# Optimization experiments

Hardware: AMD Instinct MI355X
Metric: run time of the kernel (lower is better)

The kernel has to match this reference:

```python
import jax, jax.numpy as jnp
import numpy as np

B, V = 4, 5                      # batch_size, nview
CUBE = (80, 80, 20)              # PICT_STRUCT.CUBE_SIZE
NBINS = CUBE[0] * CUBE[1] * CUBE[2]
IMG_W, IMG_H = 960, 512          # NETWORK.IMAGE_SIZE (w, h)
ORI_W, ORI_H = 1920, 1080        # NETWORK.ORI_IMAGE_SIZE
HM_W, HM_H = 240, 128            # NETWORK.HEATMAP_SIZE
C_IMG, C_FEAT = 3, 32
C_TOT = C_IMG + C_FEAT
HID = 256
D_IN = 3 + 2 * C_TOT             # points + [mean, var] volume features


def setup_inputs():
    key = jax.random.key(0)
    ks = jax.random.split(key, 10)
    denorm_imgs = jax.random.uniform(ks[0], (V, B, C_IMG, IMG_H, IMG_W), jnp.float32)
    feats2d = jax.random.normal(ks[1], (V, B, C_FEAT, HM_H, HM_W), jnp.float32)
    lo = jnp.array([-1500.0, -1500.0, -300.0], jnp.float32)
    hi = jnp.array([1500.0, 1500.0, 300.0], jnp.float32)
    grids = lo + (hi - lo) * jax.random.uniform(ks[2], (B, NBINS, 3), jnp.float32)
    # near-identity rotations, camera centers ~3m behind the volume so all
    # points project inside the original image
    R = jnp.tile(jnp.eye(3, dtype=jnp.float32), (V, B, 1, 1)) \
        + 0.01 * jax.random.normal(ks[3], (V, B, 3, 3), jnp.float32)
    T = jnp.tile(jnp.array([0.0, 0.0, -3000.0], jnp.float32).reshape(3, 1), (V, B, 1, 1)) \
        + 50.0 * jax.random.normal(ks[4], (V, B, 3, 1), jnp.float32)
    f = 1500.0 + 10.0 * jax.random.normal(ks[5], (V, B, 2), jnp.float32)
    c_cam = jnp.tile(jnp.array([ORI_W / 2.0, ORI_H / 2.0], jnp.float32), (V, B, 1))
    k_dist = jnp.zeros((V, B, 3), jnp.float32)
    p_dist = jnp.zeros((V, B, 2), jnp.float32)
    resize_transform = jnp.array([[IMG_W / ORI_W, 0.0, 0.0],
                                  [0.0, IMG_H / ORI_H, 0.0]], jnp.float32)
    s1, s2 = 1.0 / np.sqrt(D_IN), 1.0 / np.sqrt(HID)
    W1 = (s1 * jax.random.normal(ks[6], (D_IN, HID))).astype(jnp.float32)
    b1 = jnp.zeros((HID,), jnp.float32)
    W2 = (s2 * jax.random.normal(ks[7], (HID, HID))).astype(jnp.float32)
    b2 = jnp.zeros((HID,), jnp.float32)
    W3 = (s2 * jax.random.normal(ks[8], (HID, 1))).astype(jnp.float32)
    b3 = jnp.zeros((1,), jnp.float32)
    return dict(denorm_imgs=denorm_imgs, feats2d=feats2d, grids=grids, R=R, T=T,
                f=f, c_cam=c_cam, k_dist=k_dist, p_dist=p_dist,
                resize_transform=resize_transform,
                W1=W1, b1=b1, W2=W2, b2=b2, W3=W3, b3=b3)


def _project(x, R, T, f, c, k, p):
    # voxelpose project_point_radial: x [N,3] world-mm -> [N,2] pixel coords
    xcam = R @ (x.T - T)                               # [3,N]
    y = xcam[:2] / (xcam[2:3] + 1e-5)                  # [2,N]
    r2 = jnp.sum(y * y, axis=0)
    radial = 1.0 + k[0] * r2 + k[1] * r2 ** 2 + k[2] * r2 ** 3
    tan = p[0] * y[1] + p[1] * y[0]
    y = y * (radial + 2.0 * tan)[None, :] + jnp.stack([p[1], p[0]])[:, None] * r2[None, :]
    return (f[:, None] * y + c[:, None]).T             # [N,2]


def _bilinear(img, gx, gy):
    # F.grid_sample bilinear, align_corners=True, padding_mode='zeros'
    # img: [C,H,W]; gx,gy: [N] in [-1,1] -> [C,N]
    C, H, W = img.shape
    x = (gx + 1.0) * 0.5 * (W - 1)
    y = (gy + 1.0) * 0.5 * (H - 1)
    x0, y0 = jnp.floor(x), jnp.floor(y)
    wx1, wy1 = x - x0, y - y0
    wx0, wy0 = 1.0 - wx1, 1.0 - wy1

    def tap(xi, yi):
        valid = (xi >= 0) & (xi <= W - 1) & (yi >= 0) & (yi <= H - 1)
        xi_c = jnp.clip(xi.astype(jnp.int32), 0, W - 1)
        yi_c = jnp.clip(yi.astype(jnp.int32), 0, H - 1)
        return img[:, yi_c, xi_c] * valid.astype(img.dtype)

    return (tap(x0, y0) * (wx0 * wy0) + tap(x0 + 1.0, y0) * (wx1 * wy0)
            + tap(x0, y0 + 1.0) * (wx0 * wy1) + tap(x0 + 1.0, y0 + 1.0) * (wx1 * wy1))


def _sample_view(img, feat, pts, R, T, f, c, k, p, trans):
    xy = _project(pts, R, T, f, c, k, p)
    xy = jnp.clip(xy, -1.0, float(max(ORI_W, ORI_H)))
    xy = jnp.concatenate([xy, jnp.ones((xy.shape[0], 1), xy.dtype)], axis=1) @ trans.T
    g = xy / jnp.array([IMG_W - 1.0, IMG_H - 1.0], jnp.float32) * 2.0 - 1.0
    si = _bilinear(img, g[:, 0], g[:, 1])              # [C_IMG, N]
    sf = _bilinear(feat, g[:, 0], g[:, 1])             # [C_FEAT, N]
    return jnp.concatenate([si, sf], axis=0)           # [C_TOT, N]


def reference(denorm_imgs, feats2d, grids, R, T, f, c_cam, k_dist, p_dist,
              resize_transform, W1, b1, W2, b2, W3, b3):
    per_b = jax.vmap(_sample_view, in_axes=(0, 0, 0, 0, 0, 0, 0, 0, 0, None))
    per_vb = jax.vmap(per_b, in_axes=(0, 0, None, 0, 0, 0, 0, 0, 0, None))
    cubes = per_vb(denorm_imgs, feats2d, grids, R, T, f, c_cam, k_dist, p_dist,
                   resize_transform)                   # [V,B,C,N]
    cubes = jnp.transpose(cubes, (1, 2, 3, 0))         # [B,C,N,V]
    mean = jnp.mean(cubes, axis=-1)                    # sum(cubes/nview)
    var = jnp.sum((cubes - mean[..., None]) ** 2, axis=-1) / V
    var = jnp.exp(-var)
    gvol = jnp.concatenate([mean, var], axis=1)        # [B,2C,N]
    # nerf_model.query_density: MLP over (points, per-point global volume feats)
    feat = jnp.concatenate([grids / 1000.0, jnp.swapaxes(gvol, 1, 2)], axis=-1)  # [B,N,D_IN]
    h = jax.nn.relu(feat @ W1 + b1)
    h = jax.nn.relu(h @ W2 + b2)
    density = jax.nn.softplus(h @ W3 + b3)             # [B,N,1]
    alpha = 1.0 - jnp.exp(-density)
    return alpha.reshape(B, 1, CUBE[0], CUBE[1], CUBE[2])
```

## Files before the change

kernel.cpp:

```cpp
#include <hip/hip_runtime.h>

#define NVIEW 5
#define BATCH 4
#define NPTS 128000
#define CIMG 3
#define CFEAT 32
#define CTOT 35
#define DIN 73
#define HID 256
#define IMG_W 960
#define IMG_H 512
#define HM_W 240
#define HM_H 128
#define HW_IMG (IMG_W * IMG_H)
#define HW_HM (HM_W * HM_H)

#define BP 32

typedef __attribute__((ext_vector_type(8))) short bf16x8;
typedef __attribute__((ext_vector_type(4))) float f32x4;
typedef __attribute__((ext_vector_type(4))) unsigned short ushort4v;
typedef __attribute__((ext_vector_type(8))) unsigned short ushort8v;

__device__ inline unsigned short bf16_rtne(float f) {
    unsigned u = __builtin_bit_cast(unsigned, f);
    u += 0x7FFFu + ((u >> 16) & 1u);
    return (unsigned short)(u >> 16);
}
__device__ inline float bf2f(unsigned short u) {
    return __builtin_bit_cast(float, ((unsigned)u) << 16);
}

struct Tap {
    int o00, o01, o10, o11;
    float w00, w01, w10, w11;
};

__device__ inline void make_tap(float gx, float gy, int W, int H, Tap& t) {
    float x = (gx + 1.0f) * 0.5f * (float)(W - 1);
    float y = (gy + 1.0f) * 0.5f * (float)(H - 1);
    float x0 = floorf(x), y0 = floorf(y);
    float x1 = x0 + 1.0f, y1 = y0 + 1.0f;
    float wx1 = x - x0, wy1 = y - y0;
    float wx0 = 1.0f - wx1, wy0 = 1.0f - wy1;
    float vx0 = (x0 >= 0.0f && x0 <= (float)(W - 1)) ? 1.0f : 0.0f;
    float vx1 = (x1 >= 0.0f && x1 <= (float)(W - 1)) ? 1.0f : 0.0f;
    float vy0 = (y0 >= 0.0f && y0 <= (float)(H - 1)) ? 1.0f : 0.0f;
    float vy1 = (y1 >= 0.0f && y1 <= (float)(H - 1)) ? 1.0f : 0.0f;
    int ix0 = min(max((int)x0, 0), W - 1);
    int ix1 = min(max((int)x1, 0), W - 1);
    int iy0 = min(max((int)y0, 0), H - 1);
    int iy1 = min(max((int)y1, 0), H - 1);
    t.o00 = iy0 * W + ix0;  t.w00 = wx0 * wy0 * vx0 * vy0;
    t.o01 = iy0 * W + ix1;  t.w01 = wx1 * wy0 * vx1 * vy0;
    t.o10 = iy1 * W + ix0;  t.w10 = wx0 * wy1 * vx0 * vy1;
    t.o11 = iy1 * W + ix1;  t.w11 = wx1 * wy1 * vx1 * vy1;
}

__device__ inline float4 f4zero() { float4 r; r.x = r.y = r.z = r.w = 0.f; return r; }
__device__ inline float4 tapacc(ushort4v a, float w, float4 acc) {
    acc.x += w * bf2f(a[0]); acc.y += w * bf2f(a[1]);
    acc.z += w * bf2f(a[2]); acc.w += w * bf2f(a[3]); return acc;
}
__device__ inline float4 f4add(float4 a, float4 b) {
    a.x += b.x; a.y += b.y; a.z += b.z; a.w += b.w; return a;
}
__device__ inline float4 f4addsq(float4 acc, float4 v) {
    acc.x += v.x * v.x; acc.y += v.y * v.y; acc.z += v.z * v.z; acc.w += v.w * v.w; return acc;
}

__global__ __launch_bounds__(256) void transpose_img(const float* __restrict__ in,
                                                     unsigned short* __restrict__ out) {
    int idx = blockIdx.x * 256 + threadIdx.x;
    int vb = idx / (HW_IMG / 4);
    int p4 = idx - vb * (HW_IMG / 4);
    const float* src = in + (size_t)vb * 3 * HW_IMG + p4 * 4;
    float4 c0 = *reinterpret_cast<const float4*>(src);
    float4 c1 = *reinterpret_cast<const float4*>(src + HW_IMG);
    float4 c2 = *reinterpret_cast<const float4*>(src + 2 * HW_IMG);
    ushort8v o01, o23;
    o01[0] = bf16_rtne(c0.x); o01[1] = bf16_rtne(c1.x); o01[2] = bf16_rtne(c2.x); o01[3] = 0;
    o01[4] = bf16_rtne(c0.y); o01[5] = bf16_rtne(c1.y); o01[6] = bf16_rtne(c2.y); o01[7] = 0;
    o23[0] = bf16_rtne(c0.z); o23[1] = bf16_rtne(c1.z); o23[2] = bf16_rtne(c2.z); o23[3] = 0;
    o23[4] = bf16_rtne(c0.w); o23[5] = bf16_rtne(c1.w); o23[6] = bf16_rtne(c2.w); o23[7] = 0;
    ushort8v* dst = reinterpret_cast<ushort8v*>(out + ((size_t)vb * HW_IMG + p4 * 4) * 4);
    dst[0] = o01;
    dst[1] = o23;
}

__global__ __launch_bounds__(256) void transpose_feat(const float* __restrict__ in,
                                                      unsigned short* __restrict__ out) {
    int idx = blockIdx.x * 256 + threadIdx.x;
    int vb = idx / HW_HM;
    int pix = idx - vb * HW_HM;
    const float* src = in + (size_t)vb * 32 * HW_HM + pix;
    ushort8v* dst = reinterpret_cast<ushort8v*>(out + (size_t)idx * 32);
#pragma unroll
    for (int k = 0; k < 4; ++k) {
        ushort8v o;
#pragma unroll
        for (int j = 0; j < 8; ++j)
            o[j] = bf16_rtne(src[(8 * k + j) * HW_HM]);
        dst[k] = o;
    }
}

__global__ __launch_bounds__(256) void prep_weights(const float* __restrict__ W1,
                                                    const float* __restrict__ W2,
                                                    unsigned short* __restrict__ W1b,
                                                    unsigned short* __restrict__ W2b) {
    int idx = blockIdx.x * 256 + threadIdx.x;
    if (idx < 16 * 3 * 64) {
        int l = idx & 63;
        int ks = (idx >> 6) % 3;
        int nt = idx / 192;
        int n = nt * 16 + (l & 15);
        int k0 = ks * 32 + (l >> 4) * 8;
        ushort8v o;
#pragma unroll
        for (int j = 0; j < 8; ++j) {
            int k = k0 + j;
            float v = (k < DIN) ? W1[k * HID + n] : 0.0f;
            o[j] = bf16_rtne(v);
        }
        reinterpret_cast<ushort8v*>(W1b)[idx] = o;
    } else if (idx < 16 * 3 * 64 + 16 * 8 * 64) {
        int id2 = idx - 16 * 3 * 64;
        int l = id2 & 63;
        int ks = (id2 >> 6) & 7;
        int nt = id2 >> 9;
        int n = nt * 16 + (l & 15);
        int k0 = ks * 32 + (l >> 4) * 8;
        ushort8v o;
#pragma unroll
        for (int j = 0; j < 8; ++j)
            o[j] = bf16_rtne(W2[(k0 + j) * HID + n]);
        reinterpret_cast<ushort8v*>(W2b)[id2] = o;
    }
}

__global__ __launch_bounds__(256, 4) void fused_denorm_project(
    const unsigned short* __restrict__ wsImg,
    const unsigned short* __restrict__ wsFeat,
    const unsigned short* __restrict__ W1b,
    const unsigned short* __restrict__ W2b,
    const float* __restrict__ grids,
    const float* __restrict__ Rm,
    const float* __restrict__ Tm,
    const float* __restrict__ fcam,
    const float* __restrict__ ccam,
    const float* __restrict__ kdist,
    const float* __restrict__ pdist,
    const float* __restrict__ trans,
    const float* __restrict__ b1,
    const float* __restrict__ b2,
    const float* __restrict__ W3,
    const float* __restrict__ b3,
    float* __restrict__ out)
{
    __shared__ unsigned short featb[BP * 96];
    __shared__ unsigned short h1T[BP * 256];
    __shared__ float b1L[HID], b2L[HID], w3L[HID];
    __shared__ float partial[4][BP];

    const int tid = threadIdx.x;
    const int blk = blockIdx.x;
    const int b   = blk / (NPTS / BP);
    const int n0  = (blk % (NPTS / BP)) * BP;

    b1L[tid] = b1[tid];
    b2L[tid] = b2[tid];
    w3L[tid] = W3[tid];

    {
        const int t = tid & 7;
        const int p = tid >> 3;
        const int n = n0 + p;
        char* fbB = (char*)featb;
        const int rowoff = p * 192;
        const int sw = (p & 7) << 4;

        const float px = grids[(b * NPTS + n) * 3 + 0];
        const float py = grids[(b * NPTS + n) * 3 + 1];
        const float pz = grids[(b * NPTS + n) * 3 + 2];
        if (t == 1) {
            *(unsigned short*)(fbB + ((rowoff + 0) ^ sw)) = bf16_rtne(px * 1e-3f);
            *(unsigned short*)(fbB + ((rowoff + 2) ^ sw)) = bf16_rtne(py * 1e-3f);
            *(unsigned short*)(fbB + ((rowoff + 4) ^ sw)) = bf16_rtne(pz * 1e-3f);
        }
        {
            int c0 = 73 + t * 3;
            int cnt = (t == 7) ? 2 : 3;
            for (int j = 0; j < cnt; ++j)
                *(unsigned short*)(fbB + ((rowoff + (c0 + j) * 2) ^ sw)) = 0;
        }

        Tap myF = {}; Tap myI = {};
        if (t < NVIEW) {
            const int vb = t * BATCH + b;
            const float* Rp = Rm + vb * 9;
            const float* Tp = Tm + vb * 3;
            float X = px - Tp[0], Y = py - Tp[1], Z = pz - Tp[2];
            float xc = Rp[0] * X + Rp[1] * Y + Rp[2] * Z;
            float yc = Rp[3] * X + Rp[4] * Y + Rp[5] * Z;
            float zc = Rp[6] * X + Rp[7] * Y + Rp[8] * Z;
            float inv = 1.0f / (zc + 1e-5f);
            float y0 = xc * inv, y1 = yc * inv;
            float r2 = y0 * y0 + y1 * y1;
            float k0 = kdist[vb * 3 + 0], k1 = kdist[vb * 3 + 1], k2 = kdist[vb * 3 + 2];
            float p0 = pdist[vb * 2 + 0], p1 = pdist[vb * 2 + 1];
            float radial = 1.0f + r2 * (k0 + r2 * (k1 + r2 * k2));
            float tn = p0 * y1 + p1 * y0;
            float scl = radial + 2.0f * tn;
            float uu = y0 * scl + p1 * r2;
            float vv = y1 * scl + p0 * r2;
            float xo = fcam[vb * 2 + 0] * uu + ccam[vb * 2 + 0];
            float yo = fcam[vb * 2 + 1] * vv + ccam[vb * 2 + 1];
            xo = fminf(fmaxf(xo, -1.0f), 1920.0f);
            yo = fminf(fmaxf(yo, -1.0f), 1920.0f);
            float xr = trans[0] * xo + trans[1] * yo + trans[2];
            float yr = trans[3] * xo + trans[4] * yo + trans[5];
            float gx = xr * (1.0f / (float)(IMG_W - 1)) * 2.0f - 1.0f;
            float gy = yr * (1.0f / (float)(IMG_H - 1)) * 2.0f - 1.0f;
            make_tap(gx, gy, HM_W, HM_H, myF);
            make_tap(gx, gy, IMG_W, IMG_H, myI);
        }

        float4 s4 = f4zero(), q4 = f4zero();
        const int lb = (tid & 63) & 56;
        for (int v = 0; v < NVIEW; ++v) {
            const int src = lb + v;
            Tap tF;
            tF.o00 = __shfl(myF.o00, src, 64);
            tF.o01 = __shfl(myF.o01, src, 64);
            tF.o10 = __shfl(myF.o10, src, 64);
            tF.o11 = __shfl(myF.o11, src, 64);
            tF.w00 = __shfl(myF.w00, src, 64);
            tF.w01 = __shfl(myF.w01, src, 64);
            tF.w10 = __shfl(myF.w10, src, 64);
            tF.w11 = __shfl(myF.w11, src, 64);
            const unsigned short* fb = wsFeat + (size_t)(v * BATCH + b) * HW_HM * 32 + t * 4;
            ushort4v a00 = *reinterpret_cast<const ushort4v*>(fb + (size_t)tF.o00 * 32);
            ushort4v a01 = *reinterpret_cast<const ushort4v*>(fb + (size_t)tF.o01 * 32);
            ushort4v a10 = *reinterpret_cast<const ushort4v*>(fb + (size_t)tF.o10 * 32);
            ushort4v a11 = *reinterpret_cast<const ushort4v*>(fb + (size_t)tF.o11 * 32);
            float4 val = f4zero();
            val = tapacc(a00, tF.w00, val);
            val = tapacc(a01, tF.w01, val);
            val = tapacc(a10, tF.w10, val);
            val = tapacc(a11, tF.w11, val);
            s4 = f4add(s4, val);
            q4 = f4addsq(q4, val);
        }

        float4 si = f4zero(), qi = f4zero();
        if (t < NVIEW) {
            const unsigned short* ib = wsImg + (size_t)(t * BATCH + b) * HW_IMG * 4;
            ushort4v i00 = *reinterpret_cast<const ushort4v*>(ib + (size_t)myI.o00 * 4);
            ushort4v i01 = *reinterpret_cast<const ushort4v*>(ib + (size_t)myI.o01 * 4);
            ushort4v i10 = *reinterpret_cast<const ushort4v*>(ib + (size_t)myI.o10 * 4);
            ushort4v i11 = *reinterpret_cast<const ushort4v*>(ib + (size_t)myI.o11 * 4);
            float4 vi = f4zero();
            vi = tapacc(i00, myI.w00, vi);
            vi = tapacc(i01, myI.w01, vi);
            vi = tapacc(i10, myI.w10, vi);
            vi = tapacc(i11, myI.w11, vi);
            si = vi;
            qi = f4addsq(f4zero(), vi);
        }
#pragma unroll
        for (int off = 1; off <= 4; off <<= 1) {
            si.x += __shfl_xor(si.x, off, 64);
            si.y += __shfl_xor(si.y, off, 64);
            si.z += __shfl_xor(si.z, off, 64);
            qi.x += __shfl_xor(qi.x, off, 64);
            qi.y += __shfl_xor(qi.y, off, 64);
            qi.z += __shfl_xor(qi.z, off, 64);
        }

        const float inv5 = 1.0f / (float)NVIEW;
        {
            float m0 = s4.x * inv5, m1 = s4.y * inv5, m2 = s4.z * inv5, m3 = s4.w * inv5;
            int cm = 6 + 4 * t;
            int cv = 41 + 4 * t;
            *(unsigned short*)(fbB + ((rowoff + (cm + 0) * 2) ^ sw)) = bf16_rtne(m0);
            *(unsigned short*)(fbB + ((rowoff + (cm + 1) * 2) ^ sw)) = bf16_rtne(m1);
            *(unsigned short*)(fbB + ((rowoff + (cm + 2) * 2) ^ sw)) = bf16_rtne(m2);
            *(unsigned short*)(fbB + ((rowoff + (cm + 3) * 2) ^ sw)) = bf16_rtne(m3);
            *(unsigned short*)(fbB + ((rowoff + (cv + 0) * 2) ^ sw)) = bf16_rtne(expf(-(q4.x * inv5 - m0 * m0)));
            *(unsigned short*)(fbB + ((rowoff + (cv + 1) * 2) ^ sw)) = bf16_rtne(expf(-(q4.y * inv5 - m1 * m1)));
            *(unsigned short*)(fbB + ((rowoff + (cv + 2) * 2) ^ sw)) = bf16_rtne(expf(-(q4.z * inv5 - m2 * m2)));
            *(unsigned short*)(fbB + ((rowoff + (cv + 3) * 2) ^ sw)) = bf16_rtne(expf(-(q4.w * inv5 - m3 * m3)));
        }
        if (t == 0) {
            float m0 = si.x * inv5, m1 = si.y * inv5, m2 = si.z * inv5;
            *(unsigned short*)(fbB + ((rowoff + 3 * 2) ^ sw)) = bf16_rtne(m0);
            *(unsigned short*)(fbB + ((rowoff + 4 * 2) ^ sw)) = bf16_rtne(m1);
            *(unsigned short*)(fbB + ((rowoff + 5 * 2) ^ sw)) = bf16_rtne(m2);
            *(unsigned short*)(fbB + ((rowoff + 38 * 2) ^ sw)) = bf16_rtne(expf(-(qi.x * inv5 - m0 * m0)));
            *(unsigned short*)(fbB + ((rowoff + 39 * 2) ^ sw)) = bf16_rtne(expf(-(qi.y * inv5 - m1 * m1)));
            *(unsigned short*)(fbB + ((rowoff + 40 * 2) ^ sw)) = bf16_rtne(expf(-(qi.z * inv5 - m2 * m2)));
        }
    }
    __syncthreads();

    const int l   = tid & 63;
    const int w   = tid >> 6;
    const int g   = l >> 4;
    const int c16 = l & 15;

    {
        f32x4 acc[4][2];
#pragma unroll
        for (int nl = 0; nl < 4; ++nl)
#pragma unroll
            for (int pt = 0; pt < 2; ++pt) acc[nl][pt] = (f32x4)0.0f;

        const bf16x8* wfrag = reinterpret_cast<const bf16x8*>(W1b);
#pragma unroll
        for (int ks = 0; ks < 3; ++ks) {
            bf16x8 bfr[2];
#pragma unroll
            for (int pt = 0; pt < 2; ++pt) {
                int p = pt * 16 + c16;
                int off = (p * 192 + (ks * 32 + g * 8) * 2) ^ ((p & 7) << 4);
                bfr[pt] = *reinterpret_cast<const bf16x8*>((const char*)featb + off);
            }
#pragma unroll
            for (int nl = 0; nl < 4; ++nl) {
                int nt = w * 4 + nl;
                bf16x8 a = wfrag[(nt * 3 + ks) * 64 + l];
                acc[nl][0] = __builtin_amdgcn_mfma_f32_16x16x32_bf16(a, bfr[0], acc[nl][0], 0, 0, 0);
                acc[nl][1] = __builtin_amdgcn_mfma_f32_16x16x32_bf16(a, bfr[1], acc[nl][1], 0, 0, 0);
            }
        }
#pragma unroll
        for (int nl = 0; nl < 4; ++nl) {
            int nb = (w * 4 + nl) * 16 + g * 4;
            float bb0 = b1L[nb + 0], bb1 = b1L[nb + 1], bb2 = b1L[nb + 2], bb3v = b1L[nb + 3];
#pragma unroll
            for (int pt = 0; pt < 2; ++pt) {
                int p = pt * 16 + c16;
                ushort4v pk;
                pk[0] = bf16_rtne(fmaxf(acc[nl][pt][0] + bb0, 0.0f));
                pk[1] = bf16_rtne(fmaxf(acc[nl][pt][1] + bb1, 0.0f));
                pk[2] = bf16_rtne(fmaxf(acc[nl][pt][2] + bb2, 0.0f));
                pk[3] = bf16_rtne(fmaxf(acc[nl][pt][3] + bb3v, 0.0f));
                int off = (p * 512 + nb * 2) ^ ((p & 7) << 4);
                *reinterpret_cast<ushort4v*>((char*)h1T + off) = pk;
            }
        }
    }
    __syncthreads();

    {
        f32x4 acc[4][2];
#pragma unroll
        for (int nl = 0; nl < 4; ++nl)
#pragma unroll
            for (int pt = 0; pt < 2; ++pt) acc[nl][pt] = (f32x4)0.0f;

        const bf16x8* wfrag = reinterpret_cast<const bf16x8*>(W2b);
#pragma unroll
        for (int ks = 0; ks < 8; ++ks) {
            bf16x8 bfr[2];
#pragma unroll
            for (int pt = 0; pt < 2; ++pt) {
                int p = pt * 16 + c16;
                int off = (p * 512 + (ks * 32 + g * 8) * 2) ^ ((p & 7) << 4);
                bfr[pt] = *reinterpret_cast<const bf16x8*>((const char*)h1T + off);
            }
#pragma unroll
            for (int nl = 0; nl < 4; ++nl) {
                int nt = w * 4 + nl;
                bf16x8 a = wfrag[(nt * 8 + ks) * 64 + l];
                acc[nl][0] = __builtin_amdgcn_mfma_f32_16x16x32_bf16(a, bfr[0], acc[nl][0], 0, 0, 0);
                acc[nl][1] = __builtin_amdgcn_mfma_f32_16x16x32_bf16(a, bfr[1], acc[nl][1], 0, 0, 0);
            }
        }
        float s0 = 0.0f, s1 = 0.0f;
#pragma unroll
        for (int nl = 0; nl < 4; ++nl) {
            int nb = (w * 4 + nl) * 16 + g * 4;
#pragma unroll
            for (int r = 0; r < 4; ++r) {
                float b2v = b2L[nb + r];
                float w3v = w3L[nb + r];
                s0 += fmaxf(acc[nl][0][r] + b2v, 0.0f) * w3v;
                s1 += fmaxf(acc[nl][1][r] + b2v, 0.0f) * w3v;
            }
        }
        s0 += __shfl_xor(s0, 16, 64);
        s0 += __shfl_xor(s0, 32, 64);
        s1 += __shfl_xor(s1, 16, 64);
        s1 += __shfl_xor(s1, 32, 64);
        if (g == 0) {
            partial[w][c16]      = s0;
            partial[w][16 + c16] = s1;
        }
    }
    __syncthreads();

    if (tid < BP) {
        float v = partial[0][tid] + partial[1][tid] + partial[2][tid] + partial[3][tid] + b3[0];
        out[b * NPTS + n0 + tid] = 1.0f / (1.0f + expf(-v));
    }
}

extern "C" void kernel_launch(void* const* d_in, const int* in_sizes, int n_in,
                              void* d_out, int out_size, void* d_ws, size_t ws_size,
                              hipStream_t stream) {
    const float* imgs  = (const float*)d_in[0];
    const float* feats = (const float*)d_in[1];
    const float* grids = (const float*)d_in[2];
    const float* Rm    = (const float*)d_in[3];
    const float* Tm    = (const float*)d_in[4];
    const float* fcam  = (const float*)d_in[5];
    const float* ccam  = (const float*)d_in[6];
    const float* kdist = (const float*)d_in[7];
    const float* pdist = (const float*)d_in[8];
    const float* trans = (const float*)d_in[9];
    const float* W1    = (const float*)d_in[10];
    const float* b1    = (const float*)d_in[11];
    const float* W2    = (const float*)d_in[12];
    const float* b2    = (const float*)d_in[13];
    const float* W3    = (const float*)d_in[14];
    const float* b3    = (const float*)d_in[15];
    float* out = (float*)d_out;

    unsigned short* wsImg  = (unsigned short*)d_ws;
    unsigned short* wsFeat = wsImg + (size_t)NVIEW * BATCH * HW_IMG * 4;
    unsigned short* W1b    = wsFeat + (size_t)NVIEW * BATCH * HW_HM * 32;
    unsigned short* W2b    = W1b + 16 * 3 * 64 * 8;

    transpose_img<<<(NVIEW * BATCH * HW_IMG / 4) / 256, 256, 0, stream>>>(imgs, wsImg);
    transpose_feat<<<(NVIEW * BATCH * HW_HM) / 256, 256, 0, stream>>>(feats, wsFeat);
    prep_weights<<<44, 256, 0, stream>>>(W1, W2, W1b, W2b);

    const int nblocks = BATCH * (NPTS / BP);
    fused_denorm_project<<<nblocks, 256, 0, stream>>>(
        wsImg, wsFeat, W1b, W2b, grids, Rm, Tm, fcam, ccam, kdist, pdist, trans,
        b1, b2, W3, b3, out);
}
```

Before: 509.0 us.

## Merge prep kernels into one launch and raise fused kernel occupancy bound

Folds the image transpose, feature transpose and weight-packing kernels into a single prep_all kernel that dispatches on block index, cutting two kernel launches and their gaps. The main fused kernel's launch bounds move from 4 to 6 waves-per-EU hint, which pushes the compiler to use fewer registers so more blocks stay resident. This risks register spilling in the MLP/MFMA section of the fused kernel.

```diff
diff --git a/kernel.cpp b/kernel.cpp
--- a/kernel.cpp
+++ b/kernel.cpp
@@ -16,6 +16,10 @@
 #define HW_HM (HM_W * HM_H)
 
 #define BP 32
+
+#define NB_IMG  (NVIEW * BATCH * HW_IMG / 4 / 256)
+#define NB_FEAT (NVIEW * BATCH * HW_HM / 256)
+#define NB_W    44
 
 typedef __attribute__((ext_vector_type(8))) short bf16x8;
 typedef __attribute__((ext_vector_type(4))) float f32x4;
@@ -69,77 +73,78 @@
     acc.x += v.x * v.x; acc.y += v.y * v.y; acc.z += v.z * v.z; acc.w += v.w * v.w; return acc;
 }
 
-__global__ __launch_bounds__(256) void transpose_img(const float* __restrict__ in,
-                                                     unsigned short* __restrict__ out) {
-    int idx = blockIdx.x * 256 + threadIdx.x;
-    int vb = idx / (HW_IMG / 4);
-    int p4 = idx - vb * (HW_IMG / 4);
-    const float* src = in + (size_t)vb * 3 * HW_IMG + p4 * 4;
-    float4 c0 = *reinterpret_cast<const float4*>(src);
-    float4 c1 = *reinterpret_cast<const float4*>(src + HW_IMG);
-    float4 c2 = *reinterpret_cast<const float4*>(src + 2 * HW_IMG);
-    ushort8v o01, o23;
-    o01[0] = bf16_rtne(c0.x); o01[1] = bf16_rtne(c1.x); o01[2] = bf16_rtne(c2.x); o01[3] = 0;
-    o01[4] = bf16_rtne(c0.y); o01[5] = bf16_rtne(c1.y); o01[6] = bf16_rtne(c2.y); o01[7] = 0;
-    o23[0] = bf16_rtne(c0.z); o23[1] = bf16_rtne(c1.z); o23[2] = bf16_rtne(c2.z); o23[3] = 0;
-    o23[4] = bf16_rtne(c0.w); o23[5] = bf16_rtne(c1.w); o23[6] = bf16_rtne(c2.w); o23[7] = 0;
-    ushort8v* dst = reinterpret_cast<ushort8v*>(out + ((size_t)vb * HW_IMG + p4 * 4) * 4);
-    dst[0] = o01;
-    dst[1] = o23;
-}
-
-__global__ __launch_bounds__(256) void transpose_feat(const float* __restrict__ in,
-                                                      unsigned short* __restrict__ out) {
-    int idx = blockIdx.x * 256 + threadIdx.x;
-    int vb = idx / HW_HM;
-    int pix = idx - vb * HW_HM;
-    const float* src = in + (size_t)vb * 32 * HW_HM + pix;
-    ushort8v* dst = reinterpret_cast<ushort8v*>(out + (size_t)idx * 32);
-#pragma unroll
-    for (int k = 0; k < 4; ++k) {
-        ushort8v o;
-#pragma unroll
-        for (int j = 0; j < 8; ++j)
-            o[j] = bf16_rtne(src[(8 * k + j) * HW_HM]);
-        dst[k] = o;
+__global__ __launch_bounds__(256) void prep_all(const float* __restrict__ imgs,
+                                                const float* __restrict__ feats,
+                                                const float* __restrict__ W1,
+                                                const float* __restrict__ W2,
+                                                unsigned short* __restrict__ wsImg,
+                                                unsigned short* __restrict__ wsFeat,
+                                                unsigned short* __restrict__ W1b,
+                                                unsigned short* __restrict__ W2b) {
+    int blk = blockIdx.x;
+    if (blk < NB_IMG) {
+        int idx = blk * 256 + threadIdx.x;
+        int vb = idx / (HW_IMG / 4);
+        int p4 = idx - vb * (HW_IMG / 4);
+        const float* src = imgs + (size_t)vb * 3 * HW_IMG + p4 * 4;
+        float4 c0 = *reinterpret_cast<const float4*>(src);
+        float4 c1 = *reinterpret_cast<const float4*>(src + HW_IMG);
+        float4 c2 = *reinterpret_cast<const float4*>(src + 2 * HW_IMG);
+        ushort8v o01, o23;
+        o01[0] = bf16_rtne(c0.x); o01[1] = bf16_rtne(c1.x); o01[2] = bf16_rtne(c2.x); o01[3] = 0;
+        o01[4] = bf16_rtne(c0.y); o01[5] = bf16_rtne(c1.y); o01[6] = bf16_rtne(c2.y); o01[7] = 0;
+        o23[0] = bf16_rtne(c0.z); o23[1] = bf16_rtne(c1.z); o23[2] = bf16_rtne(c2.z); o23[3] = 0;
+        o23[4] = bf16_rtne(c0.w); o23[5] = bf16_rtne(c1.w); o23[6] = bf16_rtne(c2.w); o23[7] = 0;
+        ushort8v* dst = reinterpret_cast<ushort8v*>(wsImg + ((size_t)vb * HW_IMG + p4 * 4) * 4);
+        dst[0] = o01;
+        dst[1] = o23;
+    } else if (blk < NB_IMG + NB_FEAT) {
+        int idx = (blk - NB_IMG) * 256 + threadIdx.x;
+        int vb = idx / HW_HM;
+        int pix = idx - vb * HW_HM;
+        const float* src = feats + (size_t)vb * 32 * HW_HM + pix;
+        ushort8v* dst = reinterpret_cast<ushort8v*>(wsFeat + (size_t)idx * 32);
+#pragma unroll
+        for (int k = 0; k < 4; ++k) {
+            ushort8v o;
+#pragma unroll
+            for (int j = 0; j < 8; ++j)
+                o[j] = bf16_rtne(src[(8 * k + j) * HW_HM]);
+            dst[k] = o;
+        }
+    } else {
+        int idx = (blk - NB_IMG - NB_FEAT) * 256 + threadIdx.x;
+        if (idx < 16 * 3 * 64) {
+            int l = idx & 63;
+            int ks = (idx >> 6) % 3;
+            int nt = idx / 192;
+            int n = nt * 16 + (l & 15);
+            int k0 = ks * 32 + (l >> 4) * 8;
+            ushort8v o;
+#pragma unroll
+            for (int j = 0; j < 8; ++j) {
+                int k = k0 + j;
+                float v = (k < DIN) ? W1[k * HID + n] : 0.0f;
+                o[j] = bf16_rtne(v);
+            }
+            reinterpret_cast<ushort8v*>(W1b)[idx] = o;
+        } else if (idx < 16 * 3 * 64 + 16 * 8 * 64) {
+            int id2 = idx - 16 * 3 * 64;
+            int l = id2 & 63;
+            int ks = (id2 >> 6) & 7;
+            int nt = id2 >> 9;
+            int n = nt * 16 + (l & 15);
+            int k0 = ks * 32 + (l >> 4) * 8;
+            ushort8v o;
+#pragma unroll
+            for (int j = 0; j < 8; ++j)
+                o[j] = bf16_rtne(W2[(k0 + j) * HID + n]);
+            reinterpret_cast<ushort8v*>(W2b)[id2] = o;
+        }
     }
 }
 
-__global__ __launch_bounds__(256) void prep_weights(const float* __restrict__ W1,
-                                                    const float* __restrict__ W2,
-                                                    unsigned short* __restrict__ W1b,
-                                                    unsigned short* __restrict__ W2b) {
-    int idx = blockIdx.x * 256 + threadIdx.x;
-    if (idx < 16 * 3 * 64) {
-        int l = idx & 63;
-        int ks = (idx >> 6) % 3;
-        int nt = idx / 192;
-        int n = nt * 16 + (l & 15);
-        int k0 = ks * 32 + (l >> 4) * 8;
-        ushort8v o;
-#pragma unroll
-        for (int j = 0; j < 8; ++j) {
-            int k = k0 + j;
-            float v = (k < DIN) ? W1[k * HID + n] : 0.0f;
-            o[j] = bf16_rtne(v);
-        }
-        reinterpret_cast<ushort8v*>(W1b)[idx] = o;
-    } else if (idx < 16 * 3 * 64 + 16 * 8 * 64) {
-        int id2 = idx - 16 * 3 * 64;
-        int l = id2 & 63;
-        int ks = (id2 >> 6) & 7;
-        int nt = id2 >> 9;
-        int n = nt * 16 + (l & 15);
-        int k0 = ks * 32 + (l >> 4) * 8;
-        ushort8v o;
-#pragma unroll
-        for (int j = 0; j < 8; ++j)
-            o[j] = bf16_rtne(W2[(k0 + j) * HID + n]);
-        reinterpret_cast<ushort8v*>(W2b)[id2] = o;
-    }
-}
-
-__global__ __launch_bounds__(256, 4) void fused_denorm_project(
+__global__ __launch_bounds__(256, 6) void fused_denorm_project(
     const unsigned short* __restrict__ wsImg,
     const unsigned short* __restrict__ wsFeat,
     const unsigned short* __restrict__ W1b,
@@ -433,9 +438,8 @@
     unsigned short* W1b    = wsFeat + (size_t)NVIEW * BATCH * HW_HM * 32;
     unsigned short* W2b    = W1b + 16 * 3 * 64 * 8;
 
-    transpose_img<<<(NVIEW * BATCH * HW_IMG / 4) / 256, 256, 0, stream>>>(imgs, wsImg);
-    transpose_feat<<<(NVIEW * BATCH * HW_HM) / 256, 256, 0, stream>>>(feats, wsFeat);
-    prep_weights<<<44, 256, 0, stream>>>(W1, W2, W1b, W2b);
+    prep_all<<<NB_IMG + NB_FEAT + NB_W, 256, 0, stream>>>(
+        imgs, feats, W1, W2, wsImg, wsFeat, W1b, W2b);
 
     const int nblocks = BATCH * (NPTS / BP);
     fused_denorm_project<<<nblocks, 256, 0, stream>>>(
```

Measured after the change: 490.4 us. 3.7% less time.
